# Performance work log

Hardware: AMD Instinct MI355X
Metric: run time of the kernel (lower is better)

Reference implementation:

```python
import jax, jax.numpy as jnp
import numpy as np

B, S, D, H, DFF = 2, 4096, 512, 8, 2048
DK = D // H
EPS = 1e-6


def layer_norm(x, alpha, bias):
    # torch: (x - mean) / (std + eps), std unbiased (ddof=1), eps added to std
    mean = jnp.mean(x, axis=-1, keepdims=True)
    std = jnp.std(x, axis=-1, keepdims=True, ddof=1)
    return alpha * (x - mean) / (std + EPS) + bias


def setup_inputs() -> dict:
    key = jax.random.key(0)
    ks = jax.random.split(key, 10)
    s = 0.02
    return {
        "x": jax.random.normal(ks[0], (B, S, D), jnp.float32),
        "mask": jax.random.randint(ks[1], (S, S), 0, 2, jnp.int32),
        "w_q": jax.random.normal(ks[2], (D, D), jnp.float32) * s,
        "w_k": jax.random.normal(ks[3], (D, D), jnp.float32) * s,
        "w_v": jax.random.normal(ks[4], (D, D), jnp.float32) * s,
        "w_o": jax.random.normal(ks[5], (D, D), jnp.float32) * s,
        "w1": jax.random.normal(ks[6], (D, DFF), jnp.float32) * s,
        "b1": jnp.zeros((DFF,), jnp.float32),
        "w2": jax.random.normal(ks[7], (DFF, D), jnp.float32) * s,
        "b2": jnp.zeros((D,), jnp.float32),
        "ln1_a": jnp.ones((D,), jnp.float32),
        "ln1_b": jnp.zeros((D,), jnp.float32),
        "ln2_a": jnp.ones((D,), jnp.float32),
        "ln2_b": jnp.zeros((D,), jnp.float32),
    }


def reference(x, mask, w_q, w_k, w_v, w_o, w1, b1, w2, b2, ln1_a, ln1_b, ln2_a, ln2_b):
    # --- sublayer 0: pre-norm self-attention with residual (dropout=0/eval) ---
    h = layer_norm(x, ln1_a, ln1_b)                       # [B,S,D]
    q = (h @ w_q).reshape(B, S, H, DK)
    k = (h @ w_k).reshape(B, S, H, DK)
    v = (h @ w_v).reshape(B, S, H, DK)
    scores = jnp.einsum("bqhd,bkhd->bhqk", q, k) / jnp.sqrt(jnp.float32(DK))
    scores = jnp.where(mask[None, None, :, :] == 0, jnp.float32(-1e9), scores)
    attn = jax.nn.softmax(scores, axis=-1)                # [B,H,S,S]
    ctx = jnp.einsum("bhqk,bkhd->bqhd", attn, v).reshape(B, S, D)
    x = x + ctx @ w_o
    # --- sublayer 1: pre-norm FFN with residual ---
    h2 = layer_norm(x, ln2_a, ln2_b)
    ff = jax.nn.relu(h2 @ w1 + b1) @ w2 + b2
    return x + ff
```

## Files before the change

kernel.cpp:

```cpp
#include <hip/hip_runtime.h>
#include <hip/hip_bf16.h>
#include <stdint.h>

#define S_LEN 4096
#define DMODEL 512
#define NHEAD 8
#define DHEAD 64
#define NTOK 8192

typedef unsigned short ushort_t;
typedef __attribute__((ext_vector_type(8))) short short8;
typedef __attribute__((ext_vector_type(4))) float f32x4;
typedef unsigned long long u64;
typedef __attribute__((ext_vector_type(2))) unsigned uint2v;

__device__ __forceinline__ float bf2f(ushort_t h) {
    union { unsigned u; float f; } c; c.u = ((unsigned)h) << 16; return c.f;
}
__device__ __forceinline__ ushort_t f2bf(float f) {
    union { float f; unsigned u; } c; c.f = f;
    unsigned u = c.u + 0x7fffu + ((c.u >> 16) & 1u);
    return (ushort_t)(u >> 16);
}
__device__ __forceinline__ void glds16(const ushort_t* g, ushort_t* l) {
    __builtin_amdgcn_global_load_lds(
        (const __attribute__((address_space(1))) unsigned int*)g,
        (__attribute__((address_space(3))) unsigned int*)l, 16, 0, 0);
}

__global__ __launch_bounds__(256) void maskbits_kernel(const int* __restrict__ mask,
        u64* __restrict__ mb) {
    size_t id = (size_t)blockIdx.x * 256 + threadIdx.x;
    int v = mask[id];
    u64 bits = __ballot(v != 0);
    if ((threadIdx.x & 63) == 0) mb[id >> 6] = bits;
}

__global__ __launch_bounds__(256) void wtrans_all(const float* __restrict__ wq,
        const float* __restrict__ wk, const float* __restrict__ wv,
        const float* __restrict__ wo, const float* __restrict__ w1,
        const float* __restrict__ w2,
        ushort_t* wqT, ushort_t* wkT, ushort_t* wvT, ushort_t* woT,
        ushort_t* w1T, ushort_t* w2T) {
    __shared__ __attribute__((aligned(16))) ushort_t t[64][72];
    int z = blockIdx.z;
    const float* src; ushort_t* dst; int R, C;
    switch (z) {
        case 0: src = wq; dst = wqT; R = 512;  C = 512;  break;
        case 1: src = wk; dst = wkT; R = 512;  C = 512;  break;
        case 2: src = wv; dst = wvT; R = 512;  C = 512;  break;
        case 3: src = wo; dst = woT; R = 512;  C = 512;  break;
        case 4: src = w1; dst = w1T; R = 512;  C = 2048; break;
        default: src = w2; dst = w2T; R = 2048; C = 512; break;
    }
    int r0 = blockIdx.x * 64, c0 = blockIdx.y * 64;
    if (r0 >= R || c0 >= C) return;
    int tid = threadIdx.x;
    for (int i = tid; i < 4096; i += 256) {
        int r = i >> 6, c = i & 63;
        t[r][c] = f2bf(src[(size_t)(r0 + r) * C + c0 + c]);
    }
    __syncthreads();
    for (int i = tid; i < 512; i += 256) {
        int c = i >> 3, rb = i & 7;
        short8 vv;
#pragma unroll
        for (int j = 0; j < 8; j++) ((ushort_t*)&vv)[j] = t[rb * 8 + j][c];
        *(short8*)(dst + (size_t)(c0 + c) * R + r0 + rb * 8) = vv;
    }
}

__global__ __launch_bounds__(256) void ln_f32(const float* __restrict__ x,
        const float* __restrict__ ga, const float* __restrict__ be,
        ushort_t* __restrict__ out) {
    int tok = blockIdx.x * 4 + (threadIdx.x >> 6);
    int lane = threadIdx.x & 63;
    const float* xr = x + (size_t)tok * DMODEL + lane * 8;
    f32x4 v0 = *(const f32x4*)xr;
    f32x4 v1 = *(const f32x4*)(xr + 4);
    float f[8];
    float s = 0.f, s2 = 0.f;
#pragma unroll
    for (int i = 0; i < 8; i++) {
        f[i] = (i < 4) ? v0[i] : v1[i - 4];
        s += f[i]; s2 += f[i] * f[i];
    }
#pragma unroll
    for (int off = 1; off < 64; off <<= 1) {
        s += __shfl_xor(s, off);
        s2 += __shfl_xor(s2, off);
    }
    float mean = s * (1.f / DMODEL);
    float var = (s2 - (float)DMODEL * mean * mean) * (1.f / (DMODEL - 1));
    var = fmaxf(var, 0.f);
    float inv = 1.f / (sqrtf(var) + 1e-6f);
    short8 o;
#pragma unroll
    for (int i = 0; i < 8; i++) {
        float val = ga[lane * 8 + i] * (f[i] - mean) * inv + be[lane * 8 + i];
        ((ushort_t*)&o)[i] = f2bf(val);
    }
    *(short8*)(out + (size_t)tok * DMODEL + lane * 8) = o;
}

__global__ __launch_bounds__(256) void vtrans(const ushort_t* __restrict__ V,
        ushort_t* __restrict__ VT) {
    __shared__ __attribute__((aligned(16))) ushort_t t[64][72];
    int s0 = blockIdx.x * 64;
    int bh = blockIdx.y;
    int b = bh >> 3, h = bh & 7;
    int tid = threadIdx.x;
    const ushort_t* src = V + ((size_t)b * S_LEN + s0) * DMODEL + h * DHEAD;
    for (int i = tid; i < 512; i += 256) {
        int r = i >> 3, cb = i & 7;
        *(short8*)&t[r][cb * 8] = *(const short8*)(src + (size_t)r * DMODEL + cb * 8);
    }
    __syncthreads();
    ushort_t* dst = VT + (size_t)bh * DHEAD * S_LEN;
    for (int i = tid; i < 512; i += 256) {
        int d = i >> 3, rb = i & 7;
        short8 vv;
#pragma unroll
        for (int j = 0; j < 8; j++) ((ushort_t*)&vv)[j] = t[rb * 8 + j][d];
        *(short8*)(dst + (size_t)d * S_LEN + s0 + rb * 8) = vv;
    }
}

template <int MW, int NW>
__device__ __forceinline__ void gemm_body(const ushort_t* __restrict__ A,
        const ushort_t* __restrict__ BT, void* __restrict__ C,
        int N, int K, float scale, const float* __restrict__ bias,
        const float* __restrict__ res, int relu, int cf32,
        ushort_t* As, ushort_t* Bs, int m0, int n0, int aoff, int coff) {
    int tid = threadIdx.x;
    int wave = tid >> 6, lane = tid & 63;
    int wm = wave >> 1, wn = wave & 1;
    int lr = lane & 15, lg = lane >> 4;
    int srow = lane >> 2, spos = lane & 3;
    int swz = (spos ^ ((srow >> 1) & 3)) * 8;
    int rdw = (lr >> 1) & 3;
    f32x4 acc[MW][NW];
#pragma unroll
    for (int i = 0; i < MW; i++)
#pragma unroll
        for (int j = 0; j < NW; j++) acc[i][j] = (f32x4){0.f, 0.f, 0.f, 0.f};

    const ushort_t* Ag = A + (size_t)(m0 - aoff) * K;
    const ushort_t* Bg = BT + (size_t)n0 * K;

    for (int k0 = 0; k0 < K; k0 += 32) {
        __syncthreads();
        for (int ia = wave; ia < 2 * MW; ia += 4)
            glds16(Ag + (size_t)(ia * 16 + srow) * K + k0 + swz, As + ia * 16 * 32);
        for (int ib = wave; ib < 2 * NW; ib += 4)
            glds16(Bg + (size_t)(ib * 16 + srow) * K + k0 + swz, Bs + ib * 16 * 32);
        __syncthreads();
        short8 af[MW], bfv[NW];
#pragma unroll
        for (int t = 0; t < MW; t++)
            af[t] = *(const short8*)(As + (wm * 16 * MW + t * 16 + lr) * 32 + (lg ^ rdw) * 8);
#pragma unroll
        for (int t = 0; t < NW; t++)
            bfv[t] = *(const short8*)(Bs + (wn * 16 * NW + t * 16 + lr) * 32 + (lg ^ rdw) * 8);
#pragma unroll
        for (int i = 0; i < MW; i++)
#pragma unroll
            for (int j = 0; j < NW; j++)
                acc[i][j] = __builtin_amdgcn_mfma_f32_16x16x32_bf16(af[i], bfv[j], acc[i][j], 0, 0, 0);
    }
#pragma unroll
    for (int i = 0; i < MW; i++) {
        int row = m0 + wm * 16 * MW + i * 16 + lg * 4;
#pragma unroll
        for (int j = 0; j < NW; j++) {
            int col = n0 + wn * 16 * NW + j * 16 + lr;
            float bb = bias ? bias[col] : 0.f;
#pragma unroll
            for (int r = 0; r < 4; r++) {
                float v = acc[i][j][r] * scale + bb;
                if (relu) v = fmaxf(v, 0.f);
                if (res) v += res[(size_t)(row + r) * N + col];
                size_t cidx = (size_t)(row + r - coff) * N + col;
                if (cf32) ((float*)C)[cidx] = v;
                else      ((ushort_t*)C)[cidx] = f2bf(v);
            }
        }
    }
}

__global__ __launch_bounds__(256) void gemm_bt64(const ushort_t* __restrict__ A,
        const ushort_t* __restrict__ BT, void* __restrict__ C,
        int N, int K, float scale, const float* bias, const float* res, int relu,
        int cf32, int m_base, int aoff, int coff) {
    __shared__ __attribute__((aligned(16))) ushort_t As[64 * 32];
    __shared__ __attribute__((aligned(16))) ushort_t Bs[64 * 32];
    gemm_body<2, 2>(A, BT, C, N, K, scale, bias, res, relu, cf32, As, Bs,
                    m_base + blockIdx.x * 64, blockIdx.y * 64, aoff, coff);
}

__global__ __launch_bounds__(256) void gemm_qkv(const ushort_t* __restrict__ A,
        const ushort_t* __restrict__ wqT, const ushort_t* __restrict__ wkT,
        const ushort_t* __restrict__ wvT,
        ushort_t* __restrict__ Q, ushort_t* __restrict__ Kb, ushort_t* __restrict__ V) {
    __shared__ __attribute__((aligned(16))) ushort_t As[128 * 32];
    __shared__ __attribute__((aligned(16))) ushort_t Bs[128 * 32];
    int z = blockIdx.z;
    const ushort_t* W = (z == 0) ? wqT : ((z == 1) ? wkT : wvT);
    ushort_t* O = (z == 0) ? Q : ((z == 1) ? Kb : V);
    float sc = (z == 0) ? 0.18033688011112042f : 1.f;
    gemm_body<4, 4>(A, W, O, DMODEL, DMODEL, sc, nullptr, nullptr, 0, 0, As, Bs,
                    blockIdx.x * 128, blockIdx.y * 128, 0, 0);
}

__global__ __launch_bounds__(128) void attn_kernel(const ushort_t* __restrict__ Q,
        const ushort_t* __restrict__ K, const ushort_t* __restrict__ VT,
        const unsigned* __restrict__ mb32, ushort_t* __restrict__ ctx) {
    __shared__ __attribute__((aligned(16))) ushort_t Ks[2][32 * 64];
    __shared__ __attribute__((aligned(16))) ushort_t Vs[2][64 * 32];
    __shared__ __attribute__((aligned(16))) ushort_t Pw[2][16 * 40];
    int qt = blockIdx.x, h = blockIdx.y, b = blockIdx.z;
    int tid = threadIdx.x;
    int wv = __builtin_amdgcn_readfirstlane(tid >> 6);
    int lane = tid & 63;
    int lr = lane & 15, lg = lane >> 4;
    size_t tokbase = (size_t)b * S_LEN;
    int q0 = qt * 32 + wv * 16;

    const ushort_t* Qp = Q + (tokbase + q0) * DMODEL + h * DHEAD;
    short8 qf0 = *(const short8*)(Qp + (size_t)lr * DMODEL + lg * 8);
    short8 qf1 = *(const short8*)(Qp + (size_t)lr * DMODEL + 32 + lg * 8);
    f32x4 o[4];
#pragma unroll
    for (int td = 0; td < 4; td++) o[td] = (f32x4){0.f, 0.f, 0.f, 0.f};
    float lsl = 0.f;

    int srow = lane >> 3, spos = lane & 7;
    int srow2 = lane >> 2, spos2 = lane & 3;
    int kst = (spos ^ srow) * 8;
    int vst = (spos2 ^ ((srow2 >> 1) & 3)) * 8;
    int rdk = lr & 7;
    int rdv = (lr >> 1) & 3;

    const ushort_t* kgl = K + tokbase * DMODEL + h * DHEAD + (size_t)srow * DMODEL + kst;
    const ushort_t* vgl = VT + (size_t)(b * NHEAD + h) * DHEAD * S_LEN
                          + (size_t)srow2 * S_LEN + vst;
    const unsigned* mr = mb32 + (size_t)(q0 + lr) * 128;

    unsigned w = mr[0];
    if (wv == 0) {
        glds16(kgl + (size_t)0 * DMODEL, &Ks[0][0 * 64]);
        glds16(kgl + (size_t)8 * DMODEL, &Ks[0][8 * 64]);
        glds16(vgl + (size_t)0 * S_LEN, &Vs[0][0 * 32]);
        glds16(vgl + (size_t)16 * S_LEN, &Vs[0][16 * 32]);
    } else {
        glds16(kgl + (size_t)16 * DMODEL, &Ks[0][16 * 64]);
        glds16(kgl + (size_t)24 * DMODEL, &Ks[0][24 * 64]);
        glds16(vgl + (size_t)32 * S_LEN, &Vs[0][32 * 32]);
        glds16(vgl + (size_t)48 * S_LEN, &Vs[0][48 * 32]);
    }

#pragma unroll 1
    for (int kt = 0; kt < S_LEN / 32; kt++) {
        int cur = kt & 1;
        __builtin_amdgcn_s_barrier();
        unsigned nw = 0;
        if (kt + 1 < S_LEN / 32) {
            nw = mr[kt + 1];
            const ushort_t* kgn = kgl + (size_t)(kt + 1) * 32 * DMODEL;
            const ushort_t* vgn = vgl + (kt + 1) * 32;
            if (wv == 0) {
                glds16(kgn + (size_t)0 * DMODEL, &Ks[cur ^ 1][0 * 64]);
                glds16(kgn + (size_t)8 * DMODEL, &Ks[cur ^ 1][8 * 64]);
                glds16(vgn + (size_t)0 * S_LEN, &Vs[cur ^ 1][0 * 32]);
                glds16(vgn + (size_t)16 * S_LEN, &Vs[cur ^ 1][16 * 32]);
            } else {
                glds16(kgn + (size_t)16 * DMODEL, &Ks[cur ^ 1][16 * 64]);
                glds16(kgn + (size_t)24 * DMODEL, &Ks[cur ^ 1][24 * 64]);
                glds16(vgn + (size_t)32 * S_LEN, &Vs[cur ^ 1][32 * 32]);
                glds16(vgn + (size_t)48 * S_LEN, &Vs[cur ^ 1][48 * 32]);
            }
            __builtin_amdgcn_s_waitcnt(3957);
        } else {
            __builtin_amdgcn_s_waitcnt(3952);
        }
        __builtin_amdgcn_s_barrier();
        const ushort_t* Kb_ = Ks[cur];
        const ushort_t* Vb_ = Vs[cur];
        f32x4 s[2];
#pragma unroll
        for (int t = 0; t < 2; t++) {
            const ushort_t* kr = Kb_ + (t * 16 + lr) * 64;
            short8 kf0 = *(const short8*)(kr + ((lg ^ rdk) * 8));
            short8 kf1 = *(const short8*)(kr + (((lg + 4) ^ rdk) * 8));
            f32x4 z = (f32x4){0.f, 0.f, 0.f, 0.f};
            z = __builtin_amdgcn_mfma_f32_16x16x32_bf16(kf0, qf0, z, 0, 0, 0);
            z = __builtin_amdgcn_mfma_f32_16x16x32_bf16(kf1, qf1, z, 0, 0, 0);
            s[t] = z;
        }
        unsigned wq = w >> (lg * 4);
#pragma unroll
        for (int r = 0; r < 4; r++) {
            float p0, p1;
            asm("v_exp_f32 %0, %1\n\ts_nop 0" : "=v"(p0) : "v"(s[0][r]));
            asm("v_exp_f32 %0, %1\n\ts_nop 0" : "=v"(p1) : "v"(s[1][r]));
            p0 = ((wq >> r) & 1u) ? p0 : 0.f;
            p1 = ((wq >> (16 + r)) & 1u) ? p1 : 0.f;
            s[0][r] = p0; s[1][r] = p1;
            lsl += p0 + p1;
        }
        ushort_t* Pb = Pw[wv];
#pragma unroll
        for (int t = 0; t < 2; t++) {
            uint2v pk;
            asm("v_cvt_pk_bf16_f32 %0, %1, %2" : "=v"(pk.x) : "v"(s[t][0]), "v"(s[t][1]));
            asm("v_cvt_pk_bf16_f32 %0, %1, %2" : "=v"(pk.y) : "v"(s[t][2]), "v"(s[t][3]));
            *(uint2v*)(Pb + lr * 40 + t * 16 + lg * 4) = pk;
        }
        short8 pf = *(const short8*)(Pb + lr * 40 + lg * 8);
#pragma unroll
        for (int td = 0; td < 4; td++) {
            short8 vf = *(const short8*)(Vb_ + (td * 16 + lr) * 32 + ((lg ^ rdv) * 8));
            o[td] = __builtin_amdgcn_mfma_f32_16x16x32_bf16(pf, vf, o[td], 0, 0, 0);
        }
        w = nw;
    }
    lsl += __shfl_xor(lsl, 16);
    lsl += __shfl_xor(lsl, 32);
    float linv = 1.f / lsl;
    float l0 = __shfl(linv, lg * 4 + 0);
    float l1 = __shfl(linv, lg * 4 + 1);
    float l2 = __shfl(linv, lg * 4 + 2);
    float l3 = __shfl(linv, lg * 4 + 3);
    size_t rowb = (tokbase + q0 + lg * 4) * DMODEL + h * DHEAD;
#pragma unroll
    for (int td = 0; td < 4; td++) {
        int cc = td * 16 + lr;
        ctx[rowb + 0 * DMODEL + cc] = f2bf(o[td][0] * l0);
        ctx[rowb + 1 * DMODEL + cc] = f2bf(o[td][1] * l1);
        ctx[rowb + 2 * DMODEL + cc] = f2bf(o[td][2] * l2);
        ctx[rowb + 3 * DMODEL + cc] = f2bf(o[td][3] * l3);
    }
}

extern "C" void kernel_launch(void* const* d_in, const int* in_sizes, int n_in,
                              void* d_out, int out_size, void* d_ws, size_t ws_size,
                              hipStream_t stream) {
    (void)in_sizes; (void)n_in; (void)out_size; (void)ws_size;
    const float* x    = (const float*)d_in[0];
    const int*   mask = (const int*)d_in[1];
    const float* w_q  = (const float*)d_in[2];
    const float* w_k  = (const float*)d_in[3];
    const float* w_v  = (const float*)d_in[4];
    const float* w_o  = (const float*)d_in[5];
    const float* w1   = (const float*)d_in[6];
    const float* b1   = (const float*)d_in[7];
    const float* w2   = (const float*)d_in[8];
    const float* b2   = (const float*)d_in[9];
    const float* l1a  = (const float*)d_in[10];
    const float* l1b  = (const float*)d_in[11];
    const float* l2a  = (const float*)d_in[12];
    const float* l2b  = (const float*)d_in[13];

    char* ws = (char*)d_ws;
    const size_t MB = 1024 * 1024;
    const size_t KB = 1024;
    ushort_t* w1T  = (ushort_t*)(ws + 0);
    ushort_t* w2T  = (ushort_t*)(ws + 2 * MB);
    ushort_t* wqT  = (ushort_t*)(ws + 4 * MB);
    ushort_t* wkT  = (ushort_t*)(ws + 4 * MB + 512 * KB);
    ushort_t* wvT  = (ushort_t*)(ws + 5 * MB);
    ushort_t* woT  = (ushort_t*)(ws + 5 * MB + 512 * KB);
    ushort_t* ff1  = (ushort_t*)(ws + 6 * MB);
    ushort_t* h    = (ushort_t*)(ws + 22 * MB);
    ushort_t* VTb  = h;
    ushort_t* h2   = h;
    ushort_t* Qb   = (ushort_t*)(ws + 30 * MB);
    float*    x2f  = (float*)(ws + 30 * MB);
    ushort_t* Kb   = (ushort_t*)(ws + 38 * MB);
    ushort_t* Vb   = (ushort_t*)(ws + 46 * MB);
    ushort_t* ctx  = Vb;
    u64*      mb   = (u64*)d_out;
    float*    out  = (float*)d_out;

    dim3 blk(256);
    maskbits_kernel<<<dim3(65536), blk, 0, stream>>>(mask, mb);
    wtrans_all<<<dim3(32, 32, 6), blk, 0, stream>>>(w_q, w_k, w_v, w_o, w1, w2,
            wqT, wkT, wvT, woT, w1T, w2T);
    ln_f32<<<dim3(NTOK / 4), blk, 0, stream>>>(x, l1a, l1b, h);
    gemm_qkv<<<dim3(64, 4, 3), blk, 0, stream>>>(h, wqT, wkT, wvT, Qb, Kb, Vb);
    vtrans<<<dim3(64, 16), blk, 0, stream>>>(Vb, VTb);
    attn_kernel<<<dim3(128, 8, 2), dim3(128), 0, stream>>>(Qb, Kb, VTb,
            (const unsigned*)mb, ctx);
    gemm_bt64<<<dim3(128, 8), blk, 0, stream>>>(ctx, woT, x2f, 512, 512, 1.f,
            nullptr, x, 0, 1, 0, 0, 0);
    ln_f32<<<dim3(NTOK / 4), blk, 0, stream>>>(x2f, l2a, l2b, h2);
    gemm_bt64<<<dim3(64, 32), blk, 0, stream>>>(h2, w1T, ff1, 2048, 512, 1.f,
            b1, nullptr, 1, 0, 0, 0, 0);
    gemm_bt64<<<dim3(64, 8), blk, 0, stream>>>(ff1, w2T, out, 512, 2048, 1.f,
            b2, x2f, 0, 1, 0, 0, 0);
    gemm_bt64<<<dim3(64, 32), blk, 0, stream>>>(h2, w1T, ff1, 2048, 512, 1.f,
            b1, nullptr, 1, 0, 4096, 0, 4096);
    gemm_bt64<<<dim3(64, 8), blk, 0, stream>>>(ff1, w2T, out, 512, 2048, 1.f,
            b2, x2f, 0, 1, 4096, 4096, 0);
}
```

Baseline: 448.7 us.

## Split attention over key halves and double query rows per wave

Each attention wave now handles 32 query rows instead of 16, so every K/V tile brought into LDS feeds twice as many MFMAs and the per-tile barriers are amortised. The key range is split into two halves across blocks, which keeps the grid size unchanged. Each half writes unnormalised bf16 partial outputs and row sums into reused workspace, and a new combine kernel adds them and normalises. The cost is extra register pressure, an extra launch, about 24 MB of extra global traffic, and a slight precision loss from storing the unnormalised partials in bf16.

Measured after the change: 453.9 us. No clear change (+1.2%).

```diff
diff --git a/kernel.cpp b/kernel.cpp
--- a/kernel.cpp
+++ b/kernel.cpp
@@ -212,27 +212,36 @@
                     blockIdx.x * 128, blockIdx.y * 128, 0, 0);
 }
 
-__global__ __launch_bounds__(128) void attn_kernel(const ushort_t* __restrict__ Q,
+__global__ __launch_bounds__(128, 4) void attn_kernel(const ushort_t* __restrict__ Q,
         const ushort_t* __restrict__ K, const ushort_t* __restrict__ VT,
-        const unsigned* __restrict__ mb32, ushort_t* __restrict__ ctx) {
+        const unsigned* __restrict__ mb32, ushort_t* __restrict__ Opart,
+        float* __restrict__ lpart) {
     __shared__ __attribute__((aligned(16))) ushort_t Ks[2][32 * 64];
     __shared__ __attribute__((aligned(16))) ushort_t Vs[2][64 * 32];
-    __shared__ __attribute__((aligned(16))) ushort_t Pw[2][16 * 40];
-    int qt = blockIdx.x, h = blockIdx.y, b = blockIdx.z;
+    __shared__ __attribute__((aligned(16))) ushort_t Pw[2][32 * 40];
+    int qt = blockIdx.x, h = blockIdx.y, zz = blockIdx.z;
+    int b = zz >> 1, half = zz & 1;
     int tid = threadIdx.x;
     int wv = __builtin_amdgcn_readfirstlane(tid >> 6);
     int lane = tid & 63;
     int lr = lane & 15, lg = lane >> 4;
     size_t tokbase = (size_t)b * S_LEN;
-    int q0 = qt * 32 + wv * 16;
+    int q0 = qt * 64 + wv * 32;
+    int k0 = half * (S_LEN / 2);
 
     const ushort_t* Qp = Q + (tokbase + q0) * DMODEL + h * DHEAD;
-    short8 qf0 = *(const short8*)(Qp + (size_t)lr * DMODEL + lg * 8);
-    short8 qf1 = *(const short8*)(Qp + (size_t)lr * DMODEL + 32 + lg * 8);
-    f32x4 o[4];
-#pragma unroll
-    for (int td = 0; td < 4; td++) o[td] = (f32x4){0.f, 0.f, 0.f, 0.f};
-    float lsl = 0.f;
+    short8 qf[2][2];
+#pragma unroll
+    for (int u = 0; u < 2; u++) {
+        qf[u][0] = *(const short8*)(Qp + (size_t)(u * 16 + lr) * DMODEL + lg * 8);
+        qf[u][1] = *(const short8*)(Qp + (size_t)(u * 16 + lr) * DMODEL + 32 + lg * 8);
+    }
+    f32x4 o[2][4];
+#pragma unroll
+    for (int u = 0; u < 2; u++)
+#pragma unroll
+        for (int td = 0; td < 4; td++) o[u][td] = (f32x4){0.f, 0.f, 0.f, 0.f};
+    float lsl[2] = {0.f, 0.f};
 
     int srow = lane >> 3, spos = lane & 7;
     int srow2 = lane >> 2, spos2 = lane & 3;
@@ -241,12 +250,14 @@
     int rdk = lr & 7;
     int rdv = (lr >> 1) & 3;
 
-    const ushort_t* kgl = K + tokbase * DMODEL + h * DHEAD + (size_t)srow * DMODEL + kst;
+    const ushort_t* kgl = K + (tokbase + k0) * DMODEL + h * DHEAD
+                          + (size_t)srow * DMODEL + kst;
     const ushort_t* vgl = VT + (size_t)(b * NHEAD + h) * DHEAD * S_LEN
-                          + (size_t)srow2 * S_LEN + vst;
-    const unsigned* mr = mb32 + (size_t)(q0 + lr) * 128;
-
-    unsigned w = mr[0];
+                          + (size_t)srow2 * S_LEN + k0 + vst;
+    const unsigned* mr0 = mb32 + (size_t)(q0 + lr) * 128 + half * 64;
+    const unsigned* mr1 = mb32 + (size_t)(q0 + 16 + lr) * 128 + half * 64;
+
+    unsigned w0 = mr0[0], w1 = mr1[0];
     if (wv == 0) {
         glds16(kgl + (size_t)0 * DMODEL, &Ks[0][0 * 64]);
         glds16(kgl + (size_t)8 * DMODEL, &Ks[0][8 * 64]);
@@ -259,13 +270,15 @@
         glds16(vgl + (size_t)48 * S_LEN, &Vs[0][48 * 32]);
     }
 
+    const int NIT = (S_LEN / 2) / 32;
 #pragma unroll 1
-    for (int kt = 0; kt < S_LEN / 32; kt++) {
+    for (int kt = 0; kt < NIT; kt++) {
         int cur = kt & 1;
         __builtin_amdgcn_s_barrier();
-        unsigned nw = 0;
-        if (kt + 1 < S_LEN / 32) {
-            nw = mr[kt + 1];
+        unsigned nw0 = 0, nw1 = 0;
+        if (kt + 1 < NIT) {
+            nw0 = mr0[kt + 1];
+            nw1 = mr1[kt + 1];
             const ushort_t* kgn = kgl + (size_t)(kt + 1) * 32 * DMODEL;
             const ushort_t* vgn = vgl + (kt + 1) * 32;
             if (wv == 0) {
@@ -279,67 +292,109 @@
                 glds16(vgn + (size_t)32 * S_LEN, &Vs[cur ^ 1][32 * 32]);
                 glds16(vgn + (size_t)48 * S_LEN, &Vs[cur ^ 1][48 * 32]);
             }
-            __builtin_amdgcn_s_waitcnt(3957);
+            __builtin_amdgcn_s_waitcnt(3958);
         } else {
             __builtin_amdgcn_s_waitcnt(3952);
         }
         __builtin_amdgcn_s_barrier();
         const ushort_t* Kb_ = Ks[cur];
         const ushort_t* Vb_ = Vs[cur];
-        f32x4 s[2];
+        f32x4 s[2][2];
 #pragma unroll
         for (int t = 0; t < 2; t++) {
             const ushort_t* kr = Kb_ + (t * 16 + lr) * 64;
             short8 kf0 = *(const short8*)(kr + ((lg ^ rdk) * 8));
             short8 kf1 = *(const short8*)(kr + (((lg + 4) ^ rdk) * 8));
-            f32x4 z = (f32x4){0.f, 0.f, 0.f, 0.f};
-            z = __builtin_amdgcn_mfma_f32_16x16x32_bf16(kf0, qf0, z, 0, 0, 0);
-            z = __builtin_amdgcn_mfma_f32_16x16x32_bf16(kf1, qf1, z, 0, 0, 0);
-            s[t] = z;
-        }
-        unsigned wq = w >> (lg * 4);
-#pragma unroll
-        for (int r = 0; r < 4; r++) {
-            float p0, p1;
-            asm("v_exp_f32 %0, %1\n\ts_nop 0" : "=v"(p0) : "v"(s[0][r]));
-            asm("v_exp_f32 %0, %1\n\ts_nop 0" : "=v"(p1) : "v"(s[1][r]));
-            p0 = ((wq >> r) & 1u) ? p0 : 0.f;
-            p1 = ((wq >> (16 + r)) & 1u) ? p1 : 0.f;
-            s[0][r] = p0; s[1][r] = p1;
-            lsl += p0 + p1;
+#pragma unroll
+            for (int u = 0; u < 2; u++) {
+                f32x4 z = (f32x4){0.f, 0.f, 0.f, 0.f};
+                z = __builtin_amdgcn_mfma_f32_16x16x32_bf16(kf0, qf[u][0], z, 0, 0, 0);
+                z = __builtin_amdgcn_mfma_f32_16x16x32_bf16(kf1, qf[u][1], z, 0, 0, 0);
+                s[t][u] = z;
+            }
+        }
+#pragma unroll
+        for (int u = 0; u < 2; u++) {
+            unsigned wq = (u ? w1 : w0) >> (lg * 4);
+#pragma unroll
+            for (int r = 0; r < 4; r++) {
+                float p0, p1;
+                asm("v_exp_f32 %0, %1\n\ts_nop 0" : "=v"(p0) : "v"(s[0][u][r]));
+                asm("v_exp_f32 %0, %1\n\ts_nop 0" : "=v"(p1) : "v"(s[1][u][r]));
+                p0 = ((wq >> r) & 1u) ? p0 : 0.f;
+                p1 = ((wq >> (16 + r)) & 1u) ? p1 : 0.f;
+                s[0][u][r] = p0; s[1][u][r] = p1;
+                lsl[u] += p0 + p1;
+            }
         }
         ushort_t* Pb = Pw[wv];
 #pragma unroll
-        for (int t = 0; t < 2; t++) {
-            uint2v pk;
-            asm("v_cvt_pk_bf16_f32 %0, %1, %2" : "=v"(pk.x) : "v"(s[t][0]), "v"(s[t][1]));
-            asm("v_cvt_pk_bf16_f32 %0, %1, %2" : "=v"(pk.y) : "v"(s[t][2]), "v"(s[t][3]));
-            *(uint2v*)(Pb + lr * 40 + t * 16 + lg * 4) = pk;
-        }
-        short8 pf = *(const short8*)(Pb + lr * 40 + lg * 8);
+        for (int u = 0; u < 2; u++)
+#pragma unroll
+            for (int t = 0; t < 2; t++) {
+                uint2v pk;
+                asm("v_cvt_pk_bf16_f32 %0, %1, %2" : "=v"(pk.x) : "v"(s[t][u][0]), "v"(s[t][u][1]));
+                asm("v_cvt_pk_bf16_f32 %0, %1, %2" : "=v"(pk.y) : "v"(s[t][u][2]), "v"(s[t][u][3]));
+                *(uint2v*)(Pb + (u * 16 + lr) * 40 + t * 16 + lg * 4) = pk;
+            }
+        short8 vf[4];
+#pragma unroll
+        for (int td = 0; td < 4; td++)
+            vf[td] = *(const short8*)(Vb_ + (td * 16 + lr) * 32 + ((lg ^ rdv) * 8));
+#pragma unroll
+        for (int u = 0; u < 2; u++) {
+            short8 pf = *(const short8*)(Pb + (u * 16 + lr) * 40 + lg * 8);
+#pragma unroll
+            for (int td = 0; td < 4; td++)
+                o[u][td] = __builtin_amdgcn_mfma_f32_16x16x32_bf16(pf, vf[td], o[u][td], 0, 0, 0);
+        }
+        w0 = nw0; w1 = nw1;
+    }
+#pragma unroll
+    for (int u = 0; u < 2; u++) {
+        lsl[u] += __shfl_xor(lsl[u], 16);
+        lsl[u] += __shfl_xor(lsl[u], 32);
+    }
+    float* lp = lpart + (size_t)half * (NHEAD * 2 * S_LEN)
+                + (size_t)(b * NHEAD + h) * S_LEN + q0;
+    if (lane < 16) {
+        lp[lane] = lsl[0];
+        lp[16 + lane] = lsl[1];
+    }
+    ushort_t* Op = Opart + (size_t)half * NTOK * DMODEL;
+#pragma unroll
+    for (int u = 0; u < 2; u++) {
+        size_t rowb = (tokbase + q0 + u * 16 + lg * 4) * DMODEL + h * DHEAD;
 #pragma unroll
         for (int td = 0; td < 4; td++) {
-            short8 vf = *(const short8*)(Vb_ + (td * 16 + lr) * 32 + ((lg ^ rdv) * 8));
-            o[td] = __builtin_amdgcn_mfma_f32_16x16x32_bf16(pf, vf, o[td], 0, 0, 0);
-        }
-        w = nw;
-    }
-    lsl += __shfl_xor(lsl, 16);
-    lsl += __shfl_xor(lsl, 32);
-    float linv = 1.f / lsl;
-    float l0 = __shfl(linv, lg * 4 + 0);
-    float l1 = __shfl(linv, lg * 4 + 1);
-    float l2 = __shfl(linv, lg * 4 + 2);
-    float l3 = __shfl(linv, lg * 4 + 3);
-    size_t rowb = (tokbase + q0 + lg * 4) * DMODEL + h * DHEAD;
-#pragma unroll
-    for (int td = 0; td < 4; td++) {
-        int cc = td * 16 + lr;
-        ctx[rowb + 0 * DMODEL + cc] = f2bf(o[td][0] * l0);
-        ctx[rowb + 1 * DMODEL + cc] = f2bf(o[td][1] * l1);
-        ctx[rowb + 2 * DMODEL + cc] = f2bf(o[td][2] * l2);
-        ctx[rowb + 3 * DMODEL + cc] = f2bf(o[td][3] * l3);
-    }
+            int cc = td * 16 + lr;
+            Op[rowb + 0 * DMODEL + cc] = f2bf(o[u][td][0]);
+            Op[rowb + 1 * DMODEL + cc] = f2bf(o[u][td][1]);
+            Op[rowb + 2 * DMODEL + cc] = f2bf(o[u][td][2]);
+            Op[rowb + 3 * DMODEL + cc] = f2bf(o[u][td][3]);
+        }
+    }
+}
+
+__global__ __launch_bounds__(256) void attn_combine(const ushort_t* __restrict__ Oa,
+        const ushort_t* __restrict__ Ob, const float* __restrict__ la,
+        const float* __restrict__ lb, ushort_t* __restrict__ ctx) {
+    size_t idx = ((size_t)blockIdx.x * 256 + threadIdx.x) * 8;
+    size_t tok = idx >> 9;
+    int col = (int)(idx & 511);
+    int h = col >> 6;
+    int b = (int)(tok >> 12);
+    int q = (int)(tok & 4095);
+    size_t li = (size_t)(b * NHEAD + h) * S_LEN + q;
+    float inv = 1.f / (la[li] + lb[li]);
+    short8 va = *(const short8*)(Oa + idx);
+    short8 vb = *(const short8*)(Ob + idx);
+    short8 oo;
+#pragma unroll
+    for (int j = 0; j < 8; j++)
+        ((ushort_t*)&oo)[j] = f2bf((bf2f(((const ushort_t*)&va)[j])
+                                  + bf2f(((const ushort_t*)&vb)[j])) * inv);
+    *(short8*)(ctx + idx) = oo;
 }
 
 extern "C" void kernel_launch(void* const* d_in, const int* in_sizes, int n_in,
@@ -379,6 +434,8 @@
     ushort_t* Kb   = (ushort_t*)(ws + 38 * MB);
     ushort_t* Vb   = (ushort_t*)(ws + 46 * MB);
     ushort_t* ctx  = Vb;
+    ushort_t* Opart = ff1;
+    float*    lpart = (float*)wqT;
     u64*      mb   = (u64*)d_out;
     float*    out  = (float*)d_out;
 
@@ -389,8 +446,10 @@
     ln_f32<<<dim3(NTOK / 4), blk, 0, stream>>>(x, l1a, l1b, h);
     gemm_qkv<<<dim3(64, 4, 3), blk, 0, stream>>>(h, wqT, wkT, wvT, Qb, Kb, Vb);
     vtrans<<<dim3(64, 16), blk, 0, stream>>>(Vb, VTb);
-    attn_kernel<<<dim3(128, 8, 2), dim3(128), 0, stream>>>(Qb, Kb, VTb,
-            (const unsigned*)mb, ctx);
+    attn_kernel<<<dim3(64, 8, 4), dim3(128), 0, stream>>>(Qb, Kb, VTb,
+            (const unsigned*)mb, Opart, lpart);
+    attn_combine<<<dim3(2048), blk, 0, stream>>>(Opart,
+            Opart + (size_t)NTOK * DMODEL, lpart, lpart + NHEAD * 2 * S_LEN, ctx);
     gemm_bt64<<<dim3(128, 8), blk, 0, stream>>>(ctx, woT, x2f, 512, 512, 1.f,
             nullptr, x, 0, 1, 0, 0, 0);
     ln_f32<<<dim3(NTOK / 4), blk, 0, stream>>>(x2f, l2a, l2b, h2);
```
